# Performance work log

Hardware: AMD Instinct MI355X
Metric: run time of the kernel (lower is better)

Reference implementation:

```python
import jax, jax.numpy as jnp
import numpy as np

SEQ_LEN = 262144
N = 128  # number of event types


def setup_inputs() -> dict:
    key = jax.random.key(0)
    k_in, k_q, k_k = jax.random.split(key, 3)
    scale = 1.0 / np.sqrt(N)  # matches nn.Linear default init scale
    Input = jax.random.normal(k_in, (SEQ_LEN, N), dtype=jnp.float32)
    W_Q = jax.random.uniform(k_q, (N, N), dtype=jnp.float32, minval=-scale, maxval=scale)
    W_K = jax.random.uniform(k_k, (N, N), dtype=jnp.float32, minval=-scale, maxval=scale)
    return {"Input": Input, "W_Q": W_Q, "W_K": W_K}


def reference(Input, W_Q, W_K):
    # Original loops over one-hot type rows e_t:
    #   query_t = e_t @ W_Q.T = W_Q[:, t]
    #   keys    = Input @ W_K.T                         (S, N)
    #   aw[:,t] = softplus(keys @ query_t)
    #   Output[s,t] = aw[s,t] * sum_j Input[s,j]
    # Fused/batched form:
    keys = Input @ W_K.T                                 # (S, N)
    aw = jax.nn.softplus(keys @ W_Q)                     # (S, N), col t uses W_Q[:, t]
    row_sum = jnp.sum(Input, axis=1, keepdims=True)      # (S, 1)
    Output = aw * row_sum                                # (S, N)
    loss = jnp.mean((Output[:-1] - Input[1:]) ** 2)
    l1 = jnp.sum(jnp.abs(jax.nn.sigmoid(W_K.T @ W_Q)))
    return (loss, l1)
```

## Files before the change

### kernel.cpp

```cpp
#include <hip/hip_runtime.h>
#include <math.h>

#define S_LEN 262144
#define N 128
#define TPB 256
#define GRID 768
#define NWAVES (GRID * 4)
#define ITEMS (S_LEN / 16 * 2)

typedef __attribute__((ext_vector_type(8))) short bf16x8;
typedef __attribute__((ext_vector_type(4))) float f32x4;

__device__ __forceinline__ unsigned short f2bf(float x) {
    unsigned b = __float_as_uint(x);
    b = (b + 0x7FFF + ((b >> 16) & 1)) >> 16;
    return (unsigned short)b;
}
__device__ __forceinline__ float bf2f(unsigned short u) {
    return __uint_as_float((unsigned)u << 16);
}
__device__ __forceinline__ unsigned pack2bf(float x, float y) {
    return __builtin_amdgcn_perm(__float_as_uint(y) + 0x8000u,
                                 __float_as_uint(x) + 0x8000u, 0x07060302u);
}
__device__ __forceinline__ float wave_reduce(float v) {
    #pragma unroll
    for (int off = 32; off > 0; off >>= 1) v += __shfl_down(v, off, 64);
    return v;
}
__device__ __forceinline__ void lds_fence() {
    asm volatile("s_waitcnt lgkmcnt(0)" ::: "memory");
}

__global__ void mk_kernel(const float* __restrict__ WQ, const float* __restrict__ WK,
                          unsigned short* __restrict__ fragB, float* __restrict__ wsP,
                          float* __restrict__ out) {
    const int i = blockIdx.x;
    const int j = threadIdx.x;
    float a0 = 0.f, a1 = 0.f, a2 = 0.f, a3 = 0.f;
    #pragma unroll
    for (int r = 0; r < N; r += 4) {
        a0 = fmaf(WK[(r + 0) * N + i], WQ[(r + 0) * N + j], a0);
        a1 = fmaf(WK[(r + 1) * N + i], WQ[(r + 1) * N + j], a1);
        a2 = fmaf(WK[(r + 2) * N + i], WQ[(r + 2) * N + j], a2);
        a3 = fmaf(WK[(r + 3) * N + i], WQ[(r + 3) * N + j], a3);
    }
    const float acc = (a0 + a1) + (a2 + a3);

    const int kk = i >> 5, q = (i >> 3) & 3, jj = i & 7;
    const int ct = j >> 4, n15 = j & 15;
    fragB[((kk * 8 + ct) * 64 + (q * 16 + n15)) * 8 + jj] = f2bf(acc);

    float sg = fabsf(1.0f / (1.0f + __expf(-acc)));
    float ws = wave_reduce(sg);
    __shared__ float red[2];
    if ((j & 63) == 0) red[j >> 6] = ws;
    __syncthreads();
    if (j == 0) wsP[i] = red[0] + red[1];
    if (i == 0 && j == 0) out[0] = 0.f;
}

__global__ __launch_bounds__(TPB, 3) void main_kernel(
    const float* __restrict__ In, const unsigned short* __restrict__ fragB,
    const float* __restrict__ wsP, float* __restrict__ out, float inv_denom) {
    __shared__ unsigned short sA[4][17][132];
    __shared__ float sRed[4];

    const int tid = threadIdx.x;
    const int w = tid >> 6, lane = tid & 63;
    const int q = lane >> 4, n15 = lane & 15;
    const int gid = blockIdx.x * 4 + w;
    const int half = gid & 1;

    unsigned short (*my)[132] = sA[w];
    float lsum = 0.f;
    float4 r[8];
    float2 x;

    auto issue = [&](int item) {
        const long r0 = (long)(item >> 1) * 16;
        const float* base = In + r0 * N;
        #pragma unroll
        for (int j = 0; j < 8; ++j)
            r[j] = *(const float4*)(base + j * 256 + lane * 4);
        long rX = r0 + 16; if (rX > S_LEN - 1) rX = S_LEN - 1;
        x = *(const float2*)&In[rX * N + lane * 2];
    };

    int item = gid;
    issue(item);

    bf16x8 bF[4][4];
    #pragma unroll
    for (int c4 = 0; c4 < 4; ++c4)
        #pragma unroll
        for (int kk = 0; kk < 4; ++kk)
            bF[c4][kk] = *(const bf16x8*)&fragB[((kk * 8 + (half * 4 + c4)) * 64 + lane) * 8];

    bf16x8 bOne;
    #pragma unroll
    for (int e = 0; e < 8; ++e) bOne[e] = (short)0x3F80;

    if (blockIdx.x == 0 && w == 0) {
        float p = wsP[lane] + wsP[lane + 64];
        float s = wave_reduce(p);
        if (lane == 0) out[1] = s;
    }

    while (item < ITEMS) {
        const int next = item + NWAVES;

        #pragma unroll
        for (int j = 0; j < 8; ++j) {
            const int row = 2 * j + (lane >> 5);
            const int c = lane & 31;
            *(unsigned int*)&my[row][c * 4] = pack2bf(r[j].x, r[j].y);
            *(unsigned int*)&my[row][c * 4 + 2] = pack2bf(r[j].z, r[j].w);
        }
        *(unsigned int*)&my[16][lane * 2] = pack2bf(x.x, x.y);

        if (next < ITEMS) issue(next);

        lds_fence();

        f32x4 acc[4], aRS;
        aRS = (f32x4){0.f, 0.f, 0.f, 0.f};
        #pragma unroll
        for (int c4 = 0; c4 < 4; ++c4) acc[c4] = (f32x4){0.f, 0.f, 0.f, 0.f};
        #pragma unroll
        for (int kk = 0; kk < 4; ++kk) {
            bf16x8 a = *(const bf16x8*)&my[n15][kk * 32 + q * 8];
            aRS = __builtin_amdgcn_mfma_f32_16x16x32_bf16(a, bOne, aRS, 0, 0, 0);
            #pragma unroll
            for (int c4 = 0; c4 < 4; ++c4)
                acc[c4] = __builtin_amdgcn_mfma_f32_16x16x32_bf16(a, bF[c4][kk], acc[c4], 0, 0, 0);
        }

        const long r0 = (long)(item >> 1) * 16;
        #pragma unroll
        for (int reg = 0; reg < 4; ++reg) {
            const int row = q * 4 + reg;
            const float rs = aRS[reg];
            const long s = r0 + row;
            const bool has = (s < S_LEN - 1);
            #pragma unroll
            for (int c4 = 0; c4 < 4; ++c4) {
                const float z = acc[c4][reg];
                const float sp = fmaxf(z, 0.f) + __logf(1.0f + __expf(-fabsf(z)));
                const float o = sp * rs;
                if (has) {
                    const int col = half * 64 + c4 * 16 + n15;
                    const float d = o - bf2f(my[row + 1][col]);
                    lsum = fmaf(d, d, lsum);
                }
            }
        }

        lds_fence();
        item = next;
    }

    const float wsum = wave_reduce(lsum);
    if ((tid & 63) == 0) sRed[w] = wsum;
    __syncthreads();
    if (tid == 0) {
        float t = 0.f;
        #pragma unroll
        for (int w2 = 0; w2 < 4; ++w2) t += sRed[w2];
        atomicAdd(&out[0], t * inv_denom);
    }
}

extern "C" void kernel_launch(void* const* d_in, const int* in_sizes, int n_in,
                              void* d_out, int out_size, void* d_ws, size_t ws_size,
                              hipStream_t stream) {
    const float* In = (const float*)d_in[0];
    const float* WQ = (const float*)d_in[1];
    const float* WK = (const float*)d_in[2];
    float* out = (float*)d_out;
    unsigned short* fragB = (unsigned short*)d_ws;
    float* wsP = (float*)((char*)d_ws + 32 * 1024);

    mk_kernel<<<128, 128, 0, stream>>>(WQ, WK, fragB, wsP, out);
    const float inv = (float)(1.0 / ((double)(S_LEN - 1) * (double)N));
    main_kernel<<<GRID, TPB, 0, stream>>>(In, fragB, wsP, out, inv);
}
```

Before: 202.3 us.

## Stream input tiles directly to LDS with triple-buffered async loads

Input rows are no longer loaded into registers and repacked to bf16 in LDS. Each wave now issues global_load_lds DMA into a swizzled fp32 LDS buffer, three items deep, and converts to bf16 when reading the MFMA A fragments. The next-row target values are read as fp32 straight from LDS instead of bf16. Blocks shrink to two waves, and the vmcnt-based wait is meant to keep more loads in flight. The cost is a larger LDS footprint per wave, which limits occupancy, plus the risk of getting the hand-tuned vmcnt count wrong.

```diff
diff --git a/kernel.cpp b/kernel.cpp
--- a/kernel.cpp
+++ b/kernel.cpp
@@ -3,22 +3,24 @@
 
 #define S_LEN 262144
 #define N 128
-#define TPB 256
+#define TPB 128
 #define GRID 768
-#define NWAVES (GRID * 4)
+#define NWAVES (GRID * 2)
 #define ITEMS (S_LEN / 16 * 2)
+#define DEPTH 3
+#define STRIP_B 8192
+#define BUF_B 8704
+#define VMCNT_WAIT "s_waitcnt vmcnt(20)"
 
 typedef __attribute__((ext_vector_type(8))) short bf16x8;
 typedef __attribute__((ext_vector_type(4))) float f32x4;
+typedef __attribute__((ext_vector_type(4))) unsigned u32x4;
 
 __device__ __forceinline__ unsigned short f2bf(float x) {
     unsigned b = __float_as_uint(x);
     b = (b + 0x7FFF + ((b >> 16) & 1)) >> 16;
     return (unsigned short)b;
 }
-__device__ __forceinline__ float bf2f(unsigned short u) {
-    return __uint_as_float((unsigned)u << 16);
-}
 __device__ __forceinline__ unsigned pack2bf(float x, float y) {
     return __builtin_amdgcn_perm(__float_as_uint(y) + 0x8000u,
                                  __float_as_uint(x) + 0x8000u, 0x07060302u);
@@ -30,6 +32,16 @@
 }
 __device__ __forceinline__ void lds_fence() {
     asm volatile("s_waitcnt lgkmcnt(0)" ::: "memory");
+}
+__device__ __forceinline__ void gload_lds16(const void* g, void* l) {
+    __builtin_amdgcn_global_load_lds(
+        (const __attribute__((address_space(1))) unsigned int*)g,
+        (__attribute__((address_space(3))) unsigned int*)l, 16, 0, 0);
+}
+__device__ __forceinline__ void gload_lds4(const void* g, void* l) {
+    __builtin_amdgcn_global_load_lds(
+        (const __attribute__((address_space(1))) unsigned int*)g,
+        (__attribute__((address_space(3))) unsigned int*)l, 4, 0, 0);
 }
 
 __global__ void mk_kernel(const float* __restrict__ WQ, const float* __restrict__ WK,
@@ -60,46 +72,39 @@
     if (i == 0 && j == 0) out[0] = 0.f;
 }
 
-__global__ __launch_bounds__(TPB, 3) void main_kernel(
+#define DMA_ITEM(it, BB) do {                                                   \
+    const long _r0 = (long)((it) >> 1) * 16;                                    \
+    const char* _gb = (const char*)In + _r0 * 512;                              \
+    _Pragma("unroll")                                                           \
+    for (int _j = 0; _j < 8; ++_j)                                              \
+        gload_lds16(_gb + gofs[_j], (char*)(BB) + _j * 1024);                   \
+    long _rX = _r0 + 16; if (_rX > S_LEN - 1) _rX = S_LEN - 1;                  \
+    const float* _bx = In + _rX * N;                                            \
+    gload_lds4(_bx + lane,      (char*)(BB) + STRIP_B);                         \
+    gload_lds4(_bx + 64 + lane, (char*)(BB) + STRIP_B + 256);                   \
+} while (0)
+
+__global__ __launch_bounds__(TPB, 2) void main_kernel(
     const float* __restrict__ In, const unsigned short* __restrict__ fragB,
     const float* __restrict__ wsP, float* __restrict__ out, float inv_denom) {
-    __shared__ unsigned short sA[4][17][132];
-    __shared__ float sRed[4];
+    __shared__ __align__(16) unsigned char sBuf[2][DEPTH][BUF_B];
+    __shared__ float sRed[2];
 
     const int tid = threadIdx.x;
     const int w = tid >> 6, lane = tid & 63;
-    const int q = lane >> 4, n15 = lane & 15;
-    const int gid = blockIdx.x * 4 + w;
+    const int q = lane >> 4, n15 = lane & 15, s7 = n15 & 7;
+    const int gid = blockIdx.x * 2 + w;
     const int half = gid & 1;
 
-    unsigned short (*my)[132] = sA[w];
-    float lsum = 0.f;
-    float4 r[8];
-    float2 x;
-
-    auto issue = [&](int item) {
-        const long r0 = (long)(item >> 1) * 16;
-        const float* base = In + r0 * N;
-        #pragma unroll
-        for (int j = 0; j < 8; ++j)
-            r[j] = *(const float4*)(base + j * 256 + lane * 4);
-        long rX = r0 + 16; if (rX > S_LEN - 1) rX = S_LEN - 1;
-        x = *(const float2*)&In[rX * N + lane * 2];
-    };
-
-    int item = gid;
-    issue(item);
-
-    bf16x8 bF[4][4];
-    #pragma unroll
-    for (int c4 = 0; c4 < 4; ++c4)
-        #pragma unroll
-        for (int kk = 0; kk < 4; ++kk)
-            bF[c4][kk] = *(const bf16x8*)&fragB[((kk * 8 + (half * 4 + c4)) * 64 + lane) * 8];
-
-    bf16x8 bOne;
-    #pragma unroll
-    for (int e = 0; e < 8; ++e) bOne[e] = (short)0x3F80;
+    int gofs[8];
+    {
+        const int c = lane & 31, rowof = lane >> 5;
+        #pragma unroll
+        for (int j = 0; j < 8; ++j) {
+            const int row = j * 2 + rowof;
+            gofs[j] = row * 512 + ((c ^ (row & 7)) << 4);
+        }
+    }
 
     if (blockIdx.x == 0 && w == 0) {
         float p = wsP[lane] + wsP[lane + 64];
@@ -107,29 +112,40 @@
         if (lane == 0) out[1] = s;
     }
 
+    bf16x8 bF[4][4];
+    #pragma unroll
+    for (int c4 = 0; c4 < 4; ++c4)
+        #pragma unroll
+        for (int kk = 0; kk < 4; ++kk)
+            bF[c4][kk] = *(const bf16x8*)&fragB[((kk * 8 + (half * 4 + c4)) * 64 + lane) * 8];
+
+    bf16x8 bOne;
+    #pragma unroll
+    for (int e = 0; e < 8; ++e) bOne[e] = (short)0x3F80;
+
+    unsigned char (*bufs)[BUF_B] = sBuf[w];
+    DMA_ITEM(gid, bufs[0]);
+    DMA_ITEM(gid + NWAVES, bufs[1]);
+    DMA_ITEM(gid + 2 * NWAVES, bufs[2]);
+
+    float lsum = 0.f;
+    int item = gid, idx = 0;
     while (item < ITEMS) {
-        const int next = item + NWAVES;
-
-        #pragma unroll
-        for (int j = 0; j < 8; ++j) {
-            const int row = 2 * j + (lane >> 5);
-            const int c = lane & 31;
-            *(unsigned int*)&my[row][c * 4] = pack2bf(r[j].x, r[j].y);
-            *(unsigned int*)&my[row][c * 4 + 2] = pack2bf(r[j].z, r[j].w);
-        }
-        *(unsigned int*)&my[16][lane * 2] = pack2bf(x.x, x.y);
-
-        if (next < ITEMS) issue(next);
-
-        lds_fence();
-
-        f32x4 acc[4], aRS;
-        aRS = (f32x4){0.f, 0.f, 0.f, 0.f};
+        unsigned char* bb = bufs[idx];
+        asm volatile(VMCNT_WAIT ::: "memory");
+
+        f32x4 acc[4], aRS = (f32x4){0.f, 0.f, 0.f, 0.f};
         #pragma unroll
         for (int c4 = 0; c4 < 4; ++c4) acc[c4] = (f32x4){0.f, 0.f, 0.f, 0.f};
         #pragma unroll
         for (int kk = 0; kk < 4; ++kk) {
-            bf16x8 a = *(const bf16x8*)&my[n15][kk * 32 + q * 8];
+            const int y0 = ((kk * 8 + q * 2) ^ s7) << 4;
+            const float4 f0 = *(const float4*)(bb + n15 * 512 + y0);
+            const float4 f1 = *(const float4*)(bb + n15 * 512 + (y0 ^ 16));
+            u32x4 u;
+            u.x = pack2bf(f0.x, f0.y); u.y = pack2bf(f0.z, f0.w);
+            u.z = pack2bf(f1.x, f1.y); u.w = pack2bf(f1.z, f1.w);
+            const bf16x8 a = __builtin_bit_cast(bf16x8, u);
             aRS = __builtin_amdgcn_mfma_f32_16x16x32_bf16(a, bOne, aRS, 0, 0, 0);
             #pragma unroll
             for (int c4 = 0; c4 < 4; ++c4)
@@ -141,34 +157,37 @@
         for (int reg = 0; reg < 4; ++reg) {
             const int row = q * 4 + reg;
             const float rs = aRS[reg];
-            const long s = r0 + row;
-            const bool has = (s < S_LEN - 1);
+            const bool has = (r0 + row < S_LEN - 1);
+            const int rr = row + 1;
             #pragma unroll
             for (int c4 = 0; c4 < 4; ++c4) {
+                const int col = half * 64 + c4 * 16 + n15;
+                const int cc = col >> 2;
+                const int offS = rr * 512 + ((cc ^ (rr & 7)) << 4) + ((col & 3) << 2);
+                const int offB = STRIP_B + (col << 2);
+                const float nxv = *(const float*)(bb + (rr < 16 ? offS : offB));
                 const float z = acc[c4][reg];
                 const float sp = fmaxf(z, 0.f) + __logf(1.0f + __expf(-fabsf(z)));
                 const float o = sp * rs;
                 if (has) {
-                    const int col = half * 64 + c4 * 16 + n15;
-                    const float d = o - bf2f(my[row + 1][col]);
+                    const float d = o - nxv;
                     lsum = fmaf(d, d, lsum);
                 }
             }
         }
 
         lds_fence();
-        item = next;
+        const int nx = item + DEPTH * NWAVES;
+        if (nx < ITEMS) DMA_ITEM(nx, bb);
+
+        idx = idx + 1; if (idx == DEPTH) idx = 0;
+        item += NWAVES;
     }
 
     const float wsum = wave_reduce(lsum);
     if ((tid & 63) == 0) sRed[w] = wsum;
     __syncthreads();
-    if (tid == 0) {
-        float t = 0.f;
-        #pragma unroll
-        for (int w2 = 0; w2 < 4; ++w2) t += sRed[w2];
-        atomicAdd(&out[0], t * inv_denom);
-    }
+    if (tid == 0) atomicAdd(&out[0], (sRed[0] + sRed[1]) * inv_denom);
 }
 
 extern "C" void kernel_launch(void* const* d_in, const int* in_sizes, int n_in,
```

After: 204.5 us. No clear change (+1.1%).
